# Optimization experiments

Hardware: AMD Instinct MI355X
Metric: run time of the kernel (lower is better)

## Reference

```python
import jax, jax.numpy as jnp
import numpy as np

N = 100000   # points in scan
K = 20       # KNN neighbors
D = 96       # backbone feature dim
H = 1024     # random-projection dim
C = 7        # num classes


def setup_inputs() -> dict:
    key = jax.random.key(0)
    ks = jax.random.split(key, 6)
    feat_source = jax.random.normal(ks[0], (N, D), jnp.float32)
    proto = jax.random.normal(ks[1], (C, D), jnp.float32)
    w_rand = jax.random.normal(ks[2], (D, H), jnp.float32)
    Q = jnp.zeros((H, C), jnp.float32)
    G = jnp.zeros((H, H), jnp.float32)
    coords = jax.random.normal(ks[3], (N, 3), jnp.float32) * 30.0
    normals_z = jax.random.uniform(ks[4], (N,), jnp.float32)
    near_indices = jax.random.randint(ks[5], (N, K), 0, N).astype(jnp.int64)
    return dict(feat_source=feat_source, proto=proto, w_rand=w_rand, Q=Q, G=G,
                coords=coords, normals_z=normals_z, near_indices=near_indices)


def _prior_filter(preds, coords, normals_z):
    plane_pred = (preds == 2) | (preds == 3) | (preds == 4)
    manmade_pred = preds == 5
    other = (preds == 0) | (preds == 1) | (preds == 6)
    ground = plane_pred & (normals_z > 0.9) & (coords[:, 2] < -10.0)
    g_index = ground | other | manmade_pred
    m_index = (manmade_pred & (normals_z < 0.1)) | other | plane_pred
    return g_index, m_index


def reference(feat_source, proto, w_rand, Q, G, coords, normals_z, near_indices):
    RIDGE = 100.0  # stand-in for optimise_ridge_parameter (source not provided)
    # prototype logits: feat @ normalize(proto, dim=1).T   [N, C]
    proto_n = proto / jnp.maximum(jnp.linalg.norm(proto, axis=1, keepdims=True), 1e-12)
    pred_proto = feat_source @ proto_n.T
    preds = jnp.argmax(pred_proto, axis=1)                       # [N]
    # KNN consistency filtering (irregular gather)
    neigh = preds[near_indices]                                  # [N, K]
    consistency = jnp.mean((neigh == preds[:, None]).astype(jnp.float32), axis=1)
    cmask = consistency > 0.8
    g_index, m_index = _prior_filter(preds, coords, normals_z)
    mask = cmask & g_index & m_index                             # [N]
    # random-projection features
    feat_h = jax.nn.relu(feat_source @ w_rand)                   # [N, H]
    yhat = jax.nn.one_hot(preds, C, dtype=feat_h.dtype)          # [N, C]
    mw = mask.astype(feat_h.dtype)[:, None]
    fh_m = feat_h * mw                                           # masked rows (mask^2 == mask)
    Qn = Q + jnp.einsum('nh,nc->hc', fh_m, yhat)
    Gn = G + fh_m.T @ fh_m
    # ridge solve: wo = solve(G + r*I, Q); module does feat_h @ wo
    wo = jnp.linalg.solve(Gn + RIDGE * jnp.eye(H, dtype=Gn.dtype), Qn)  # [H, C]
    pred_domain = feat_h @ wo                                    # [N, C]
    return pred_domain
```

## Files before the change

### kernel.cpp

```cpp
#include <hip/hip_runtime.h>

#define D_DIM 96
#define K_NN  20
#define H_DIM 1024
#define C_CLS 7


__global__ void k_preds(const float* __restrict__ feat,
                        const float* __restrict__ proto,
                        const long long* __restrict__ idx_ll,
                        int* __restrict__ preds, int* __restrict__ flags, int N) {
  __shared__ float4 pn4[C_CLS * (D_DIM / 4)];
  __shared__ float inv[C_CLS];
  __shared__ int any_big;
  const int t = threadIdx.x;
  if (t == 0) any_big = 0;
  if (t < C_CLS * (D_DIM / 4)) pn4[t] = ((const float4*)proto)[t];
  if (blockIdx.x == 0) {
    for (int j = t; j < 1024; j += blockDim.x) {
      long long v = idx_ll[j];
      if (v < 0 || v >= N) any_big = 1;
    }
  }
  __syncthreads();
  if (t < C_CLS) {
    const float* row = (const float*)&pn4[t * (D_DIM / 4)];
    float ss = 0.f;
    for (int d = 0; d < D_DIM; d++) ss += row[d] * row[d];
    inv[t] = 1.0f / fmaxf(sqrtf(ss), 1e-12f);
  }
  __syncthreads();
  if (t < C_CLS * (D_DIM / 4)) {
    float s = inv[t / (D_DIM / 4)];
    float4 v = pn4[t];
    v.x *= s; v.y *= s; v.z *= s; v.w *= s;
    pn4[t] = v;
  }
  if (blockIdx.x == 0 && t == 0) {
    flags[0] = 0;
    flags[1] = any_big ? 0 : 1;
  }
  __syncthreads();

  int i = blockIdx.x * blockDim.x + t;
  int j = min(i, N - 1);
  const float4* fp = (const float4*)feat + (size_t)j * (D_DIM / 4);
  float s[C_CLS];
#pragma unroll
  for (int c = 0; c < C_CLS; c++) s[c] = 0.f;
#pragma unroll 4
  for (int q = 0; q < D_DIM / 4; q++) {
    float4 a = fp[q];
#pragma unroll
    for (int c = 0; c < C_CLS; c++) {
      float4 p = pn4[c * (D_DIM / 4) + q];
      s[c] += a.x * p.x + a.y * p.y + a.z * p.z + a.w * p.w;
    }
  }
  float best = s[0]; int bi = 0;
#pragma unroll
  for (int c = 1; c < C_CLS; c++)
    if (s[c] > best) { best = s[c]; bi = c; }
  if (i < N) preds[i] = bi;
}

__global__ void k_mask(const int* __restrict__ preds, const void* __restrict__ nearv,
                       const float* __restrict__ coords, const float* __restrict__ normz,
                       int* __restrict__ flags, int* __restrict__ list, int N) {
  int i = blockIdx.x * blockDim.x + threadIdx.x;
  if (i >= N) return;
  int p = preds[i];
  int idx[K_NN];
  if (flags[1]) {
    const longlong2* nn = (const longlong2*)((const long long*)nearv + (long long)i * K_NN);
#pragma unroll
    for (int k = 0; k < K_NN / 2; k++) {
      longlong2 v = nn[k];
      idx[2 * k] = (int)v.x; idx[2 * k + 1] = (int)v.y;
    }
  } else {
    const int4* nn = (const int4*)((const int*)nearv + (size_t)i * K_NN);
#pragma unroll
    for (int k = 0; k < K_NN / 4; k++) {
      int4 v = nn[k];
      idx[4 * k] = v.x; idx[4 * k + 1] = v.y; idx[4 * k + 2] = v.z; idx[4 * k + 3] = v.w;
    }
  }
  int cnt = 0;
#pragma unroll
  for (int k = 0; k < K_NN; k++) cnt += (preds[idx[k]] == p) ? 1 : 0;
  bool cmask = (cnt >= 17);
  bool plane = (p == 2) || (p == 3) || (p == 4);
  bool man   = (p == 5);
  bool other = (p == 0) || (p == 1) || (p == 6);
  float nz = normz[i];
  bool ground = plane && (nz > 0.9f) && (coords[(size_t)i * 3 + 2] < -10.0f);
  bool g = ground || other || man;
  bool m = (man && (nz < 0.1f)) || other || plane;
  if (cmask && g && m) {
    int pos = atomicAdd(&flags[0], 1);
    list[pos] = i;
  }
}

__device__ inline void block_reduce7(const float* val, volatile float* out,
                                     float* red) {
  int lane = threadIdx.x & 63, wave = threadIdx.x >> 6;
#pragma unroll
  for (int c = 0; c < C_CLS; c++) {
    float v = val[c];
#pragma unroll
    for (int o = 32; o > 0; o >>= 1) v += __shfl_down(v, o, 64);
    if (lane == 0) red[wave * C_CLS + c] = v;
  }
  __syncthreads();
  if (threadIdx.x == 0) {
#pragma unroll
    for (int c = 0; c < C_CLS; c++) {
      float s = 0.f;
      for (int wv = 0; wv < 16; wv++) s += red[wv * C_CLS + c];
      out[c] = s;
    }
  }
  __syncthreads();
}

__global__ void __launch_bounds__(1024) k_ridge(const float* __restrict__ feat,
                                                const float* __restrict__ w,
                                                const float* __restrict__ Q,
                                                const float* __restrict__ G,
                                                const int* __restrict__ preds,
                                                const int* __restrict__ flags,
                                                const int* __restrict__ list,
                                                float* __restrict__ Gn,
                                                float* __restrict__ wo,
                                                float* __restrict__ wo_flag) {
  const int h = threadIdx.x;
  __shared__ float psh[H_DIM * C_CLS];
  __shared__ float red[16 * C_CLS];
  __shared__ float rs[C_CLS], bn2[C_CLS], pap[C_CLS], rsn[C_CLS];

  const int M = flags[0];
  float b[C_CLS];
#pragma unroll
  for (int c = 0; c < C_CLS; c++) b[c] = Q[h * C_CLS + c];
  const float* Amat = G;
  if (M > 0) {
    for (int m = 0; m < M; m++) {
      int i = list[m];
      float s = 0.f;
      for (int d = 0; d < D_DIM; d++)
        s += feat[(size_t)i * D_DIM + d] * w[(size_t)d * H_DIM + h];
      s = fmaxf(s, 0.f);
      b[preds[i]] += s;
      psh[h] = s;
      __syncthreads();
      float sh = psh[h];
      if (m == 0) {
        for (int k = 0; k < H_DIM; k++)
          Gn[(size_t)h * H_DIM + k] = G[(size_t)h * H_DIM + k] + sh * psh[k];
      } else {
        for (int k = 0; k < H_DIM; k++)
          Gn[(size_t)h * H_DIM + k] += sh * psh[k];
      }
      __syncthreads();
    }
    Amat = Gn;
  }

  float x[C_CLS], r[C_CLS], p[C_CLS], t7[C_CLS];
#pragma unroll
  for (int c = 0; c < C_CLS; c++) {
    x[c] = 0.f; r[c] = b[c]; p[c] = b[c];
    t7[c] = b[c] * b[c];
  }
  block_reduce7(t7, rs, red);
  if (h == 0) {
#pragma unroll
    for (int c = 0; c < C_CLS; c++) bn2[c] = rs[c];
  }
  __syncthreads();

  for (int it = 0; it < H_DIM; it++) {
    bool done = true;
#pragma unroll
    for (int c = 0; c < C_CLS; c++)
      done = done && (rs[c] <= bn2[c] * 1e-16f + 1e-30f);
    if (done) break;

#pragma unroll
    for (int c = 0; c < C_CLS; c++) psh[h * C_CLS + c] = p[c];
    __syncthreads();

    float ap[C_CLS];
#pragma unroll
    for (int c = 0; c < C_CLS; c++) ap[c] = 100.0f * p[c];
    const float* grow = Amat + (size_t)h * H_DIM;
    for (int k = 0; k < H_DIM; k++) {
      float g = grow[k];
#pragma unroll
      for (int c = 0; c < C_CLS; c++) ap[c] += g * psh[k * C_CLS + c];
    }
#pragma unroll
    for (int c = 0; c < C_CLS; c++) t7[c] = p[c] * ap[c];
    block_reduce7(t7, pap, red);

    float a[C_CLS], rsold[C_CLS];
#pragma unroll
    for (int c = 0; c < C_CLS; c++) {
      rsold[c] = rs[c];
      bool act = rs[c] > bn2[c] * 1e-16f + 1e-30f;
      a[c] = act ? rsold[c] / fmaxf(pap[c], 1e-37f) : 0.f;
    }
#pragma unroll
    for (int c = 0; c < C_CLS; c++) {
      x[c] += a[c] * p[c];
      r[c] -= a[c] * ap[c];
      t7[c] = r[c] * r[c];
    }
    block_reduce7(t7, rsn, red);
#pragma unroll
    for (int c = 0; c < C_CLS; c++) {
      float bb = rsn[c] / fmaxf(rsold[c], 1e-37f);
      p[c] = r[c] + bb * p[c];
    }
    if (h == 0) {
#pragma unroll
      for (int c = 0; c < C_CLS; c++) rs[c] = rsn[c];
    }
    __syncthreads();
  }

#pragma unroll
  for (int c = 0; c < C_CLS; c++) wo[h * C_CLS + c] = x[c];
  float s = 0.f;
#pragma unroll
  for (int c = 0; c < C_CLS; c++) s += fabsf(x[c]);
  t7[0] = s;
#pragma unroll
  for (int c = 1; c < C_CLS; c++) t7[c] = 0.f;
  block_reduce7(t7, rsn, red);
  if (h == 0) *wo_flag = rsn[0];
}

__global__ void k_out(const float* __restrict__ feat, const float* __restrict__ w,
                      const float* __restrict__ wo, const float* __restrict__ wo_flag,
                      float* __restrict__ out, int N) {
  if (*wo_flag == 0.0f) {
    int total4 = (N * C_CLS) / 4;
    int stride = gridDim.x * blockDim.x;
    float4 z = make_float4(0.f, 0.f, 0.f, 0.f);
    for (int v = blockIdx.x * blockDim.x + threadIdx.x; v < total4; v += stride)
      ((float4*)out)[v] = z;
    return;
  }
  int i = blockIdx.x * blockDim.x + threadIdx.x;
  if (i >= N) return;
  float f[D_DIM];
  const float4* fp = (const float4*)(feat + (size_t)i * D_DIM);
#pragma unroll
  for (int q = 0; q < D_DIM / 4; q++) {
    float4 v = fp[q];
    f[4 * q] = v.x; f[4 * q + 1] = v.y; f[4 * q + 2] = v.z; f[4 * q + 3] = v.w;
  }
  float acc[C_CLS];
#pragma unroll
  for (int c = 0; c < C_CLS; c++) acc[c] = 0.f;
  for (int hh = 0; hh < H_DIM; hh++) {
    float s = 0.f;
#pragma unroll 8
    for (int d = 0; d < D_DIM; d++) s += f[d] * w[(size_t)d * H_DIM + hh];
    s = fmaxf(s, 0.f);
    const float* wrow = wo + hh * C_CLS;
#pragma unroll
    for (int c = 0; c < C_CLS; c++) acc[c] += s * wrow[c];
  }
#pragma unroll
  for (int c = 0; c < C_CLS; c++) out[(size_t)i * C_CLS + c] = acc[c];
}

extern "C" void kernel_launch(void* const* d_in, const int* in_sizes, int n_in,
                              void* d_out, int out_size, void* d_ws, size_t ws_size,
                              hipStream_t stream) {
  const float* feat   = (const float*)d_in[0];
  const float* proto  = (const float*)d_in[1];
  const float* w      = (const float*)d_in[2];
  const float* Q      = (const float*)d_in[3];
  const float* G      = (const float*)d_in[4];
  const float* coords = (const float*)d_in[5];
  const float* normz  = (const float*)d_in[6];
  const void*  nearv  = d_in[7];
  float* out = (float*)d_out;

  const int N = in_sizes[0] / D_DIM;

  char* WS = (char*)d_ws;
  int*   flags   = (int*)(WS + 4096);
  float* wo_flag = (float*)(WS + 4160);
  int*   preds   = (int*)(WS + 8192);
  int*   list    = (int*)(WS + 8192 + 400000);
  float* wo      = (float*)(WS + 836864);
  float* Gn      = (float*)(WS + 865536);
  if (ws_size < 5059840) return;

  int nblk = (N + 255) / 256;
  hipLaunchKernelGGL(k_preds, dim3(nblk), dim3(256), 0, stream,
                     feat, proto, (const long long*)nearv, preds, flags, N);
  hipLaunchKernelGGL(k_mask, dim3(nblk), dim3(256), 0, stream,
                     preds, nearv, coords, normz, flags, list, N);
  hipLaunchKernelGGL(k_ridge, dim3(1), dim3(1024), 0, stream,
                     feat, w, Q, G, preds, flags, list, Gn, wo, wo_flag);
  int oblk = ((N * C_CLS) / 4 + 255) / 256;
  hipLaunchKernelGGL(k_out, dim3(oblk), dim3(256), 0, stream,
                     feat, w, wo, wo_flag, out, N);
}
```

Baseline: 120.2 us.

## Fuse mask, ridge solve and output into one persistent kernel

Result: slower. 160.8 us (+33.8%).

```diff
diff --git a/kernel.cpp b/kernel.cpp
--- a/kernel.cpp
+++ b/kernel.cpp
@@ -39,6 +39,8 @@
   if (blockIdx.x == 0 && t == 0) {
     flags[0] = 0;
     flags[1] = any_big ? 0 : 1;
+    flags[2] = 0;
+    flags[3] = 0;
   }
   __syncthreads();
 
@@ -64,47 +66,8 @@
   if (i < N) preds[i] = bi;
 }
 
-__global__ void k_mask(const int* __restrict__ preds, const void* __restrict__ nearv,
-                       const float* __restrict__ coords, const float* __restrict__ normz,
-                       int* __restrict__ flags, int* __restrict__ list, int N) {
-  int i = blockIdx.x * blockDim.x + threadIdx.x;
-  if (i >= N) return;
-  int p = preds[i];
-  int idx[K_NN];
-  if (flags[1]) {
-    const longlong2* nn = (const longlong2*)((const long long*)nearv + (long long)i * K_NN);
-#pragma unroll
-    for (int k = 0; k < K_NN / 2; k++) {
-      longlong2 v = nn[k];
-      idx[2 * k] = (int)v.x; idx[2 * k + 1] = (int)v.y;
-    }
-  } else {
-    const int4* nn = (const int4*)((const int*)nearv + (size_t)i * K_NN);
-#pragma unroll
-    for (int k = 0; k < K_NN / 4; k++) {
-      int4 v = nn[k];
-      idx[4 * k] = v.x; idx[4 * k + 1] = v.y; idx[4 * k + 2] = v.z; idx[4 * k + 3] = v.w;
-    }
-  }
-  int cnt = 0;
-#pragma unroll
-  for (int k = 0; k < K_NN; k++) cnt += (preds[idx[k]] == p) ? 1 : 0;
-  bool cmask = (cnt >= 17);
-  bool plane = (p == 2) || (p == 3) || (p == 4);
-  bool man   = (p == 5);
-  bool other = (p == 0) || (p == 1) || (p == 6);
-  float nz = normz[i];
-  bool ground = plane && (nz > 0.9f) && (coords[(size_t)i * 3 + 2] < -10.0f);
-  bool g = ground || other || man;
-  bool m = (man && (nz < 0.1f)) || other || plane;
-  if (cmask && g && m) {
-    int pos = atomicAdd(&flags[0], 1);
-    list[pos] = i;
-  }
-}
-
-__device__ inline void block_reduce7(const float* val, volatile float* out,
-                                     float* red) {
+__device__ inline void reduce7_512(const float* val, volatile float* out,
+                                   float* red) {
   int lane = threadIdx.x & 63, wave = threadIdx.x >> 6;
 #pragma unroll
   for (int c = 0; c < C_CLS; c++) {
@@ -118,143 +81,225 @@
 #pragma unroll
     for (int c = 0; c < C_CLS; c++) {
       float s = 0.f;
-      for (int wv = 0; wv < 16; wv++) s += red[wv * C_CLS + c];
+      for (int wv = 0; wv < 8; wv++) s += red[wv * C_CLS + c];
       out[c] = s;
     }
   }
   __syncthreads();
 }
 
-__global__ void __launch_bounds__(1024) k_ridge(const float* __restrict__ feat,
-                                                const float* __restrict__ w,
-                                                const float* __restrict__ Q,
-                                                const float* __restrict__ G,
-                                                const int* __restrict__ preds,
-                                                const int* __restrict__ flags,
-                                                const int* __restrict__ list,
-                                                float* __restrict__ Gn,
-                                                float* __restrict__ wo,
-                                                float* __restrict__ wo_flag) {
-  const int h = threadIdx.x;
+__global__ void __launch_bounds__(512, 2)
+k_fused(const float* __restrict__ feat, const float* __restrict__ w,
+        const float* __restrict__ Q, const float* __restrict__ G,
+        const int* __restrict__ preds, const void* __restrict__ nearv,
+        const float* __restrict__ coords, const float* __restrict__ normz,
+        int* __restrict__ flags, int* __restrict__ list,
+        float* __restrict__ Gn, float* __restrict__ wo,
+        float* __restrict__ wo_flag, float* __restrict__ out, int N) {
   __shared__ float psh[H_DIM * C_CLS];
-  __shared__ float red[16 * C_CLS];
+  __shared__ float red[8 * C_CLS];
   __shared__ float rs[C_CLS], bn2[C_CLS], pap[C_CLS], rsn[C_CLS];
-
-  const int M = flags[0];
-  float b[C_CLS];
-#pragma unroll
-  for (int c = 0; c < C_CLS; c++) b[c] = Q[h * C_CLS + c];
-  const float* Amat = G;
-  if (M > 0) {
-    for (int m = 0; m < M; m++) {
-      int i = list[m];
-      float s = 0.f;
-      for (int d = 0; d < D_DIM; d++)
-        s += feat[(size_t)i * D_DIM + d] * w[(size_t)d * H_DIM + h];
-      s = fmaxf(s, 0.f);
-      b[preds[i]] += s;
-      psh[h] = s;
+  __shared__ int s_last;
+  const int t = threadIdx.x;
+
+  {
+    int i = blockIdx.x * 512 + t;
+    if (i < N) {
+      int p = preds[i];
+      int idx[K_NN];
+      if (flags[1]) {
+        const longlong2* nn = (const longlong2*)((const long long*)nearv + (long long)i * K_NN);
+#pragma unroll
+        for (int k = 0; k < K_NN / 2; k++) {
+          longlong2 v = nn[k];
+          idx[2 * k] = (int)v.x; idx[2 * k + 1] = (int)v.y;
+        }
+      } else {
+        const int4* nn = (const int4*)((const int*)nearv + (size_t)i * K_NN);
+#pragma unroll
+        for (int k = 0; k < K_NN / 4; k++) {
+          int4 v = nn[k];
+          idx[4 * k] = v.x; idx[4 * k + 1] = v.y; idx[4 * k + 2] = v.z; idx[4 * k + 3] = v.w;
+        }
+      }
+      int cnt = 0;
+#pragma unroll
+      for (int k = 0; k < K_NN; k++) cnt += (preds[idx[k]] == p) ? 1 : 0;
+      bool cmask = (cnt >= 17);
+      bool plane = (p == 2) || (p == 3) || (p == 4);
+      bool man   = (p == 5);
+      bool other = (p == 0) || (p == 1) || (p == 6);
+      float nz = normz[i];
+      bool ground = plane && (nz > 0.9f) && (coords[(size_t)i * 3 + 2] < -10.0f);
+      bool g = ground || other || man;
+      bool m = (man && (nz < 0.1f)) || other || plane;
+      if (cmask && g && m) {
+        int pos = atomicAdd(&flags[0], 1);
+        list[pos] = i;
+      }
+    }
+  }
+  __syncthreads();
+  if (t == 0) {
+    int tick = __hip_atomic_fetch_add(&flags[2], 1, __ATOMIC_ACQ_REL,
+                                      __HIP_MEMORY_SCOPE_AGENT);
+    s_last = (tick == (int)gridDim.x - 1) ? 1 : 0;
+  }
+  __syncthreads();
+
+  if (s_last) {
+    const int M = flags[0];
+    float b[2][C_CLS];
+#pragma unroll
+    for (int j = 0; j < 2; j++) {
+      int h = t + 512 * j;
+#pragma unroll
+      for (int c = 0; c < C_CLS; c++) b[j][c] = Q[h * C_CLS + c];
+    }
+    const float* Amat = G;
+    if (M > 0) {
+      for (int m = 0; m < M; m++) {
+        int im = list[m];
+        float sv[2];
+#pragma unroll
+        for (int j = 0; j < 2; j++) {
+          int h = t + 512 * j;
+          float s = 0.f;
+          for (int d = 0; d < D_DIM; d++)
+            s += feat[(size_t)im * D_DIM + d] * w[(size_t)d * H_DIM + h];
+          s = fmaxf(s, 0.f);
+          sv[j] = s;
+          b[j][preds[im]] += s;
+          psh[h] = s;
+        }
+        __syncthreads();
+#pragma unroll
+        for (int j = 0; j < 2; j++) {
+          int h = t + 512 * j;
+          float sh = sv[j];
+          float* grow = Gn + (size_t)h * H_DIM;
+          const float* g0 = G + (size_t)h * H_DIM;
+          if (m == 0) { for (int k = 0; k < H_DIM; k++) grow[k] = g0[k] + sh * psh[k]; }
+          else        { for (int k = 0; k < H_DIM; k++) grow[k] += sh * psh[k]; }
+        }
+        __syncthreads();
+      }
+      Amat = Gn;
+    }
+
+    float x[2][C_CLS], r[2][C_CLS], p[2][C_CLS], t7[C_CLS];
+#pragma unroll
+    for (int c = 0; c < C_CLS; c++) t7[c] = 0.f;
+#pragma unroll
+    for (int j = 0; j < 2; j++)
+#pragma unroll
+      for (int c = 0; c < C_CLS; c++) {
+        x[j][c] = 0.f; r[j][c] = b[j][c]; p[j][c] = b[j][c];
+        t7[c] += b[j][c] * b[j][c];
+      }
+    reduce7_512(t7, rs, red);
+    if (t == 0) {
+#pragma unroll
+      for (int c = 0; c < C_CLS; c++) bn2[c] = rs[c];
+    }
+    __syncthreads();
+
+    for (int it = 0; it < H_DIM; it++) {
+      bool done = true;
+#pragma unroll
+      for (int c = 0; c < C_CLS; c++)
+        done = done && (rs[c] <= bn2[c] * 1e-16f + 1e-30f);
+      if (done) break;
+
+#pragma unroll
+      for (int j = 0; j < 2; j++)
+#pragma unroll
+        for (int c = 0; c < C_CLS; c++) psh[(t + 512 * j) * C_CLS + c] = p[j][c];
       __syncthreads();
-      float sh = psh[h];
-      if (m == 0) {
-        for (int k = 0; k < H_DIM; k++)
-          Gn[(size_t)h * H_DIM + k] = G[(size_t)h * H_DIM + k] + sh * psh[k];
-      } else {
-        for (int k = 0; k < H_DIM; k++)
-          Gn[(size_t)h * H_DIM + k] += sh * psh[k];
+
+      float ap[2][C_CLS];
+#pragma unroll
+      for (int j = 0; j < 2; j++) {
+#pragma unroll
+        for (int c = 0; c < C_CLS; c++) ap[j][c] = 100.0f * p[j][c];
+        const float* grow = Amat + (size_t)(t + 512 * j) * H_DIM;
+        for (int k = 0; k < H_DIM; k++) {
+          float g = grow[k];
+#pragma unroll
+          for (int c = 0; c < C_CLS; c++) ap[j][c] += g * psh[k * C_CLS + c];
+        }
+      }
+#pragma unroll
+      for (int c = 0; c < C_CLS; c++)
+        t7[c] = p[0][c] * ap[0][c] + p[1][c] * ap[1][c];
+      reduce7_512(t7, pap, red);
+
+      float a[C_CLS], rsold[C_CLS];
+#pragma unroll
+      for (int c = 0; c < C_CLS; c++) {
+        rsold[c] = rs[c];
+        bool act = rs[c] > bn2[c] * 1e-16f + 1e-30f;
+        a[c] = act ? rsold[c] / fmaxf(pap[c], 1e-37f) : 0.f;
+        t7[c] = 0.f;
+      }
+#pragma unroll
+      for (int j = 0; j < 2; j++)
+#pragma unroll
+        for (int c = 0; c < C_CLS; c++) {
+          x[j][c] += a[c] * p[j][c];
+          r[j][c] -= a[c] * ap[j][c];
+          t7[c] += r[j][c] * r[j][c];
+        }
+      reduce7_512(t7, rsn, red);
+#pragma unroll
+      for (int c = 0; c < C_CLS; c++) {
+        float bb = rsn[c] / fmaxf(rsold[c], 1e-37f);
+#pragma unroll
+        for (int j = 0; j < 2; j++) p[j][c] = r[j][c] + bb * p[j][c];
+      }
+      if (t == 0) {
+#pragma unroll
+        for (int c = 0; c < C_CLS; c++) rs[c] = rsn[c];
       }
       __syncthreads();
     }
-    Amat = Gn;
-  }
-
-  float x[C_CLS], r[C_CLS], p[C_CLS], t7[C_CLS];
-#pragma unroll
-  for (int c = 0; c < C_CLS; c++) {
-    x[c] = 0.f; r[c] = b[c]; p[c] = b[c];
-    t7[c] = b[c] * b[c];
-  }
-  block_reduce7(t7, rs, red);
-  if (h == 0) {
-#pragma unroll
-    for (int c = 0; c < C_CLS; c++) bn2[c] = rs[c];
-  }
-  __syncthreads();
-
-  for (int it = 0; it < H_DIM; it++) {
-    bool done = true;
-#pragma unroll
-    for (int c = 0; c < C_CLS; c++)
-      done = done && (rs[c] <= bn2[c] * 1e-16f + 1e-30f);
-    if (done) break;
-
-#pragma unroll
-    for (int c = 0; c < C_CLS; c++) psh[h * C_CLS + c] = p[c];
+
+#pragma unroll
+    for (int c = 0; c < C_CLS; c++) t7[c] = 0.f;
+#pragma unroll
+    for (int j = 0; j < 2; j++) {
+      int h = t + 512 * j;
+#pragma unroll
+      for (int c = 0; c < C_CLS; c++) {
+        wo[h * C_CLS + c] = x[j][c];
+        t7[0] += fabsf(x[j][c]);
+      }
+    }
+#pragma unroll
+    for (int c = 1; c < C_CLS; c++) t7[c] = 0.f;
+    reduce7_512(t7, rsn, red);
+    if (t == 0) *wo_flag = rsn[0];
     __syncthreads();
-
-    float ap[C_CLS];
-#pragma unroll
-    for (int c = 0; c < C_CLS; c++) ap[c] = 100.0f * p[c];
-    const float* grow = Amat + (size_t)h * H_DIM;
-    for (int k = 0; k < H_DIM; k++) {
-      float g = grow[k];
-#pragma unroll
-      for (int c = 0; c < C_CLS; c++) ap[c] += g * psh[k * C_CLS + c];
-    }
-#pragma unroll
-    for (int c = 0; c < C_CLS; c++) t7[c] = p[c] * ap[c];
-    block_reduce7(t7, pap, red);
-
-    float a[C_CLS], rsold[C_CLS];
-#pragma unroll
-    for (int c = 0; c < C_CLS; c++) {
-      rsold[c] = rs[c];
-      bool act = rs[c] > bn2[c] * 1e-16f + 1e-30f;
-      a[c] = act ? rsold[c] / fmaxf(pap[c], 1e-37f) : 0.f;
-    }
-#pragma unroll
-    for (int c = 0; c < C_CLS; c++) {
-      x[c] += a[c] * p[c];
-      r[c] -= a[c] * ap[c];
-      t7[c] = r[c] * r[c];
-    }
-    block_reduce7(t7, rsn, red);
-#pragma unroll
-    for (int c = 0; c < C_CLS; c++) {
-      float bb = rsn[c] / fmaxf(rsold[c], 1e-37f);
-      p[c] = r[c] + bb * p[c];
-    }
-    if (h == 0) {
-#pragma unroll
-      for (int c = 0; c < C_CLS; c++) rs[c] = rsn[c];
+    if (t == 0)
+      __hip_atomic_store(&flags[3], 1, __ATOMIC_RELEASE, __HIP_MEMORY_SCOPE_AGENT);
+  } else {
+    if (t == 0) {
+      while (__hip_atomic_load(&flags[3], __ATOMIC_ACQUIRE,
+                               __HIP_MEMORY_SCOPE_AGENT) == 0)
+        __builtin_amdgcn_s_sleep(8);
     }
     __syncthreads();
   }
 
-#pragma unroll
-  for (int c = 0; c < C_CLS; c++) wo[h * C_CLS + c] = x[c];
-  float s = 0.f;
-#pragma unroll
-  for (int c = 0; c < C_CLS; c++) s += fabsf(x[c]);
-  t7[0] = s;
-#pragma unroll
-  for (int c = 1; c < C_CLS; c++) t7[c] = 0.f;
-  block_reduce7(t7, rsn, red);
-  if (h == 0) *wo_flag = rsn[0];
-}
-
-__global__ void k_out(const float* __restrict__ feat, const float* __restrict__ w,
-                      const float* __restrict__ wo, const float* __restrict__ wo_flag,
-                      float* __restrict__ out, int N) {
   if (*wo_flag == 0.0f) {
     int total4 = (N * C_CLS) / 4;
     int stride = gridDim.x * blockDim.x;
     float4 z = make_float4(0.f, 0.f, 0.f, 0.f);
-    for (int v = blockIdx.x * blockDim.x + threadIdx.x; v < total4; v += stride)
+    for (int v = blockIdx.x * 512 + t; v < total4; v += stride)
       ((float4*)out)[v] = z;
     return;
   }
-  int i = blockIdx.x * blockDim.x + threadIdx.x;
+  int i = blockIdx.x * 512 + t;
   if (i >= N) return;
   float f[D_DIM];
   const float4* fp = (const float4*)(feat + (size_t)i * D_DIM);
@@ -306,11 +351,7 @@
   int nblk = (N + 255) / 256;
   hipLaunchKernelGGL(k_preds, dim3(nblk), dim3(256), 0, stream,
                      feat, proto, (const long long*)nearv, preds, flags, N);
-  hipLaunchKernelGGL(k_mask, dim3(nblk), dim3(256), 0, stream,
-                     preds, nearv, coords, normz, flags, list, N);
-  hipLaunchKernelGGL(k_ridge, dim3(1), dim3(1024), 0, stream,
-                     feat, w, Q, G, preds, flags, list, Gn, wo, wo_flag);
-  int oblk = ((N * C_CLS) / 4 + 255) / 256;
-  hipLaunchKernelGGL(k_out, dim3(oblk), dim3(256), 0, stream,
-                     feat, w, wo, wo_flag, out, N);
+  hipLaunchKernelGGL(k_fused, dim3(256), dim3(512), 0, stream,
+                     feat, w, Q, G, preds, nearv, coords, normz,
+                     flags, list, Gn, wo, wo_flag, out, N);
 }
```
